# Kernel optimization log

Hardware: AMD Instinct MI355X
Metric: run time of the kernel (lower is better)

Reference implementation:

```python
import jax, jax.numpy as jnp
import numpy as np

N = 100000      # nodes
E = 320000      # edges
D = 128         # num_node_in_embeddings
DE = 256        # num_edge_in_embeddings = 2*D
NOBJ = 160
NREL = 27
BN_EPS = 1e-5   # eval-mode BatchNorm with running_mean=0, running_var=1


def setup_inputs() -> dict:
    key = jax.random.key(0)
    ks = jax.random.split(key, 24)
    f32 = jnp.float32
    def rn(k, shape, scale=0.05):
        return jax.random.normal(k, shape, f32) * scale
    return {
        "node_feats": jax.random.normal(ks[0], (N, D), f32),
        "edge_index": jax.random.randint(ks[1], (E, 2), 0, N),
        # GCNConv layers (W: [in,out], bias)
        "gcn1_W": rn(ks[2], (D, D // 2)), "gcn1_b": rn(ks[3], (D // 2,)),
        "gcn2_W": rn(ks[4], (D // 2, D)), "gcn2_b": rn(ks[5], (D,)),
        # edge attention (Linear(DE, D//2))
        "eattn_W": rn(ks[6], (DE, D // 2)), "eattn_b": rn(ks[7], (D // 2,)),
        # node attention (Linear(D, DE//2)) and indicator reduction (Linear(DE, DE//2))
        "nattn_W": rn(ks[8], (D, DE // 2)), "nattn_b": rn(ks[9], (DE // 2,)),
        "nred_W": rn(ks[10], (DE, DE // 2)), "nred_b": rn(ks[11], (DE // 2,)),
        # edge MLPs (1x1 Conv1d == Linear)
        "emlp1_W": rn(ks[12], (DE, DE // 2)), "emlp1_b": rn(ks[13], (DE // 2,)),
        "emlp2_W": rn(ks[14], (DE // 2, DE)), "emlp2_b": rn(ks[15], (DE,)),
        # node classification head
        "nlin1_W": rn(ks[16], (D, D // 2)),
        "nbn_g": jnp.ones((D // 2,), f32) + rn(ks[17], (D // 2,)),
        "nbn_b": rn(ks[18], (D // 2,)),
        "nlin2_W": rn(ks[19], (D // 2, NOBJ)),
        # edge classification head
        "elin1_W": rn(ks[20], (DE, DE // 2)),
        "ebn_g": jnp.ones((DE // 2,), f32) + rn(ks[21], (DE // 2,)),
        "ebn_b": rn(ks[22], (DE // 2,)),
        "elin2_W": rn(ks[23], (DE // 2, NREL)),
    }


def _seg_mean(vals, idx, n):
    # torch_scatter 'mean': sum / clamp(count, 1)
    s = jax.ops.segment_sum(vals, idx, num_segments=n)
    c = jax.ops.segment_sum(jnp.ones((vals.shape[0], 1), vals.dtype), idx, num_segments=n)
    return s / jnp.maximum(c, 1.0)


def _gcn_conv(x, src, dst, W, b, n):
    # PyG GCNConv, add_self_loops=True, symmetric normalization.
    lin = x @ W
    deg = jax.ops.segment_sum(jnp.ones((src.shape[0],), x.dtype), dst, num_segments=n) + 1.0
    dis = jax.lax.rsqrt(deg)                       # deg^{-1/2}, includes self-loop
    norm = dis[src] * dis[dst]                     # per-edge norm
    agg = jax.ops.segment_sum(lin[src] * norm[:, None], dst, num_segments=n)
    return agg + lin * (dis * dis)[:, None] + b    # self-loop term + bias


def _bn_eval(x, g, b):
    # eval-mode BatchNorm1d with running_mean=0, running_var=1
    return x * (g / jnp.sqrt(1.0 + BN_EPS)) + b


def reference(node_feats, edge_index, gcn1_W, gcn1_b, gcn2_W, gcn2_b,
              eattn_W, eattn_b, nattn_W, nattn_b, nred_W, nred_b,
              emlp1_W, emlp1_b, emlp2_W, emlp2_b,
              nlin1_W, nbn_g, nbn_b, nlin2_W,
              elin1_W, ebn_g, ebn_b, elin2_W):
    n = node_feats.shape[0]
    src = edge_index[:, 0]
    dst = edge_index[:, 1]

    # edge feature init: [subject, object - subject]  -> [E, DE]
    subj = node_feats[src]
    edge_feats = jnp.concatenate([subj, node_feats[dst] - subj], axis=1)

    # edge attention -> scatter-mean indicators over rows/cols -> node gate
    edge_ind = edge_feats @ eattn_W + eattn_b            # [E, D/2]
    row = _seg_mean(edge_ind, src, n)                    # [N, D/2]
    col = _seg_mean(edge_ind, dst, n)                    # [N, D/2]
    agg_edge_indicator = jax.nn.sigmoid(row * col)

    # two GCN layers (dropout is identity in eval mode)
    h = jax.nn.relu(_gcn_conv(node_feats, src, dst, gcn1_W, gcn1_b, n)) * agg_edge_indicator
    h = jax.nn.relu(_gcn_conv(h, src, dst, gcn2_W, gcn2_b, n))           # [N, D]

    # node attention -> per-edge gate
    node_ind = jax.nn.relu(h @ nattn_W + nattn_b)                        # [N, DE/2]
    econcat = jnp.concatenate([node_ind[src], node_ind[dst]], axis=1)    # [E, DE]
    agg_node_indicator = jax.nn.sigmoid(econcat @ nred_W + nred_b)       # [E, DE/2]

    # edge MLPs (1x1 convs == linears over edges)
    ef = jax.nn.relu(edge_feats @ emlp1_W + emlp1_b) * agg_node_indicator
    ef = jax.nn.relu(ef @ emlp2_W + emlp2_b)                             # [E, DE]

    # node head: linear -> BN(eval) -> leaky_relu(0.2) -> linear -> softmax over classes
    nx = jax.nn.leaky_relu(_bn_eval(h @ nlin1_W, nbn_g, nbn_b), 0.2)
    node_logits = jax.nn.softmax(nx @ nlin2_W, axis=1)                   # [N, NOBJ]

    # edge head: note original applies softmax on dim=1 of [1,E,NREL] -> over EDGES
    ex = jax.nn.leaky_relu(_bn_eval(ef @ elin1_W, ebn_g, ebn_b), 0.2)
    edge_logits = jax.nn.softmax(ex @ elin2_W, axis=0)                   # [E, NREL]

    return (node_logits, edge_logits)
```

## Files before the change

### kernel.cpp

```cpp
#include <hip/hip_runtime.h>

#define NN 100000
#define EE 320000

typedef unsigned int uint32;
typedef __attribute__((ext_vector_type(8))) short bf16x8;
typedef __attribute__((ext_vector_type(4))) float f32x4;
typedef __attribute__((ext_vector_type(16))) float f32x16;

__device__ __forceinline__ float4 ld4(const float* p){ return *(const float4*)p; }
__device__ __forceinline__ void st4(float* p, const float4 v){ *(float4*)p = v; }
__device__ __forceinline__ float sigm(float x){ return 1.f/(1.f + expf(-x)); }
__device__ __forceinline__ short f2b(float f){
  union { float f; uint32 u; } v; v.f = f;
  uint32 r = (v.u + 0x7FFFu + ((v.u>>16)&1u)) >> 16;
  return (short)r;
}

constexpr int EM_STORE=0, EM_BRELU=1, EM_BNLK=2;

template<int K,int NOUT,int EM>
__global__ __launch_bounds__(256) void gemm_k(
    const float* __restrict__ A,
    const float* __restrict__ W, const float* __restrict__ bias,
    const float* __restrict__ bng,
    float* __restrict__ C, int M)
{
  constexpr int CN = NOUT/16;
  __shared__ float As[16][68];
  __shared__ float Ws[16][NOUT];
  const int t  = threadIdx.x;
  const int tx = t & 15, ty = t >> 4;
  const int row0 = blockIdx.x * 64;

  float acc[4][CN];
  #pragma unroll
  for (int i=0;i<4;i++)
    #pragma unroll
    for (int j=0;j<CN;j++) acc[i][j]=0.f;

  const int r_st  = t >> 2;
  const int kq_st = (t & 3) * 4;

  for (int k0=0;k0<K;k0+=16) {
    {
      float4 v = make_float4(0.f,0.f,0.f,0.f);
      const int gr = row0 + r_st;
      if (gr < M) v = ld4(A + (size_t)gr*K + k0 + kq_st);
      As[kq_st+0][r_st]=v.x; As[kq_st+1][r_st]=v.y;
      As[kq_st+2][r_st]=v.z; As[kq_st+3][r_st]=v.w;
    }
    {
      constexpr int C4 = NOUT/4;
      for (int i=t;i<16*C4;i+=256){ int kk=i/C4, c4=(i%C4)*4;
        st4(&Ws[kk][c4], ld4(W + (size_t)(k0+kk)*NOUT + c4)); }
    }
    __syncthreads();
    #pragma unroll
    for (int kk=0;kk<16;kk++){
      float a0,a1,a2,a3;
      { const float4 av = *(const float4*)&As[kk][ty*4]; a0=av.x;a1=av.y;a2=av.z;a3=av.w; }
      float b[CN];
      if constexpr ((CN & 3) == 0) {
        #pragma unroll
        for (int j4=0;j4<CN;j4+=4){
          const float4 bv = *(const float4*)&Ws[kk][tx*CN+j4];
          b[j4]=bv.x;b[j4+1]=bv.y;b[j4+2]=bv.z;b[j4+3]=bv.w; }
      } else {
        #pragma unroll
        for (int j=0;j<CN;j++) b[j]=Ws[kk][tx*CN+j];
      }
      #pragma unroll
      for (int j=0;j<CN;j++){
        acc[0][j]=fmaf(a0,b[j],acc[0][j]);
        acc[1][j]=fmaf(a1,b[j],acc[1][j]);
        acc[2][j]=fmaf(a2,b[j],acc[2][j]);
        acc[3][j]=fmaf(a3,b[j],acc[3][j]);
      }
    }
    __syncthreads();
  }

  float sc[CN], sh[CN];
  if constexpr (EM==EM_BNLK) {
    const float r_ = rsqrtf(1.f + 1e-5f);
    #pragma unroll
    for (int j=0;j<CN;j++){ int c=tx*CN+j; sc[j]=bng[c]*r_; sh[j]=bias[c]; }
  }
  #pragma unroll
  for (int i=0;i<4;i++){
    const int r  = row0 + ty*4+i;
    if (r >= M) continue;
    #pragma unroll
    for (int j=0;j<CN;j++){
      const int c = tx*CN+j;
      float v = acc[i][j];
      if constexpr (EM==EM_BRELU) v = fmaxf(v + bias[c], 0.f);
      else if constexpr (EM==EM_BNLK){ float x = fmaf(v, sc[j], sh[j]); v = (x>0.f)? x : 0.2f*x; }
      C[(size_t)r*NOUT + c] = v;
    }
  }
}

__global__ void k_hist(const int* __restrict__ eidx, int* cntS, int* cntD, int E){
  int e = blockIdx.x*256+threadIdx.x; if (e>=E) return;
  atomicAdd(&cntS[eidx[2*e]], 1);
  atomicAdd(&cntD[eidx[2*e+1]], 1);
}
__global__ void k_scan_sum(const int* __restrict__ cnt, int* bsum, int n){
  __shared__ int red[256];
  const int b=blockIdx.x, t=threadIdx.x;
  int s=0;
  for (int i=b*1024+t; i<n && i<(b+1)*1024; i+=256) s += cnt[i];
  red[t]=s; __syncthreads();
  for (int o=128;o;o>>=1){ if(t<o) red[t]+=red[t+o]; __syncthreads(); }
  if (t==0) bsum[b]=red[0];
}
__global__ void k_scan_top(int* bsum, int nb){
  __shared__ int sh[256];
  const int t=threadIdx.x;
  int v=(t<nb)?bsum[t]:0;
  sh[t]=v; __syncthreads();
  for (int o=1;o<256;o<<=1){
    int u=0; if(t>=o) u=sh[t-o];
    __syncthreads();
    sh[t]+=u;
    __syncthreads();
  }
  if (t<nb) bsum[t]=sh[t]-v;
}
__global__ void k_scan_out(const int* __restrict__ cnt, const int* __restrict__ bofs,
                           int* __restrict__ off, int n){
  __shared__ int sh[256];
  const int b=blockIdx.x, t=threadIdx.x;
  const int base=b*1024+t*4;
  int c0=0,c1=0,c2=0,c3=0;
  if(base+0<n)c0=cnt[base+0];
  if(base+1<n)c1=cnt[base+1];
  if(base+2<n)c2=cnt[base+2];
  if(base+3<n)c3=cnt[base+3];
  int s=c0+c1+c2+c3;
  sh[t]=s; __syncthreads();
  int v=s;
  for (int o=1;o<256;o<<=1){
    int u=0; if(t>=o) u=sh[t-o];
    __syncthreads();
    sh[t]+=u;
    __syncthreads();
  }
  const int tofs = sh[t]-v + bofs[b];
  if(base+0<n) off[base+0]=tofs;
  if(base+1<n) off[base+1]=tofs+c0;
  if(base+2<n) off[base+2]=tofs+c0+c1;
  if(base+3<n) off[base+3]=tofs+c0+c1+c2;
}
__global__ void k_copyoff(const int* __restrict__ off, int* __restrict__ cur, int n){
  int i=blockIdx.x*256+threadIdx.x;
  if (i<n) cur[i]=off[i];
}
__global__ void k_setend(int* offS, int* offD, int n, int E){
  if (threadIdx.x==0 && blockIdx.x==0){ offS[n]=E; offD[n]=E; }
}
__global__ void k_fill(const int* __restrict__ eidx, int* curS, int* curD,
                       int* __restrict__ csrS, int* __restrict__ csrD, int E){
  int e=blockIdx.x*256+threadIdx.x; if (e>=E) return;
  const int s=eidx[2*e], d=eidx[2*e+1];
  csrS[atomicAdd(&curS[s],1)] = d;
  csrD[atomicAdd(&curD[d],1)] = s;
}
__global__ void k_dis(const int* __restrict__ cntD, float* __restrict__ dis, int n){
  int i=blockIdx.x*256+threadIdx.x; if(i>=n)return;
  dis[i]=rsqrtf((float)cntD[i]+1.f);
}

__global__ void k_wprep(const float* __restrict__ eattnW, const float* __restrict__ gcn1W,
                        float* __restrict__ Wcat){
  int idx=blockIdx.x*256+threadIdx.x; if (idx>=128*192) return;
  int k=idx/192, c=idx-k*192;
  float v;
  if (c<64)       v = eattnW[(size_t)(128+k)*64 + c];
  else if (c<128) v = eattnW[(size_t)k*64 + (c-64)] - eattnW[(size_t)(128+k)*64 + (c-64)];
  else            v = gcn1W[(size_t)k*64 + (c-128)];
  Wcat[idx]=v;
}

template<int NC>
__global__ void k_gather(const float* __restrict__ src, int stride, int colbase,
                         const int* __restrict__ off, const int* __restrict__ csr,
                         float* __restrict__ out, int n){
  constexpr int TPN = NC/4;
  const int t=threadIdx.x;
  const int node = blockIdx.x*(256/TPN) + t/TPN; if (node>=n) return;
  const int cq = (t%TPN)*4;
  const int j1=off[node+1];
  float4 acc = make_float4(0.f,0.f,0.f,0.f);
  for (int j=off[node]; j<j1; ++j){
    const float4 v = ld4(src + (size_t)csr[j]*stride + colbase + cq);
    acc.x+=v.x; acc.y+=v.y; acc.z+=v.z; acc.w+=v.w;
  }
  st4(out + (size_t)node*NC + cq, acc);
}

__global__ void k_aei3(const float* __restrict__ TUL, const float* __restrict__ Q,
                       const float* __restrict__ S, const int* __restrict__ cntS,
                       const int* __restrict__ cntD, const float* __restrict__ bias,
                       float* __restrict__ aei, int n){
  int idx=blockIdx.x*256+threadIdx.x; if (idx>=n*16) return;
  const int i=idx>>4, cq=(idx&15)*4;
  const float cS=(float)cntS[i], cD=(float)cntD[i];
  const float iS=1.f/fmaxf(cS,1.f), iD=1.f/fmaxf(cD,1.f);
  const float* tul = TUL + (size_t)i*192;
  const float4 T4=ld4(tul+cq), U4=ld4(tul+64+cq);
  const float4 Q4=ld4(Q+(size_t)i*64+cq), S4=ld4(S+(size_t)i*64+cq), b4=ld4(bias+cq);
  float4 o;
  o.x=sigm(((cS*(U4.x+b4.x)+Q4.x)*iS) * ((cD*(T4.x+b4.x)+S4.x)*iD));
  o.y=sigm(((cS*(U4.y+b4.y)+Q4.y)*iS) * ((cD*(T4.y+b4.y)+S4.y)*iD));
  o.z=sigm(((cS*(U4.z+b4.z)+Q4.z)*iS) * ((cD*(T4.z+b4.z)+S4.z)*iD));
  o.w=sigm(((cS*(U4.w+b4.w)+Q4.w)*iS) * ((cD*(T4.w+b4.w)+S4.w)*iD));
  st4(aei + (size_t)i*64 + cq, o);
}

template<int NC, bool AEI>
__global__ void k_gcnagg(const float* __restrict__ lin, int stride, int colbase,
                         const int* __restrict__ off, const int* __restrict__ csr,
                         const float* __restrict__ dis, const float* __restrict__ aei,
                         const float* __restrict__ bias, float* __restrict__ h, int n){
  constexpr int TPN = NC/4;
  const int t=threadIdx.x;
  const int node = blockIdx.x*(256/TPN) + t/TPN; if (node>=n) return;
  const int cq = (t%TPN)*4;
  const int j1=off[node+1];
  float4 acc = make_float4(0.f,0.f,0.f,0.f);
  for (int j=off[node]; j<j1; ++j){
    const int s=csr[j];
    const float w=dis[s];
    const float4 v = ld4(lin + (size_t)s*stride + colbase + cq);
    acc.x=fmaf(v.x,w,acc.x); acc.y=fmaf(v.y,w,acc.y);
    acc.z=fmaf(v.z,w,acc.z); acc.w=fmaf(v.w,w,acc.w);
  }
  const float dn=dis[node], d2=dn*dn;
  const float4 own=ld4(lin + (size_t)node*stride + colbase + cq), b4=ld4(bias+cq);
  float4 o;
  o.x=fmaxf(fmaf(acc.x,dn,fmaf(own.x,d2,b4.x)),0.f);
  o.y=fmaxf(fmaf(acc.y,dn,fmaf(own.y,d2,b4.y)),0.f);
  o.z=fmaxf(fmaf(acc.z,dn,fmaf(own.z,d2,b4.z)),0.f);
  o.w=fmaxf(fmaf(acc.w,dn,fmaf(own.w,d2,b4.w)),0.f);
  if (AEI){ const float4 m=ld4(aei+(size_t)node*NC+cq); o.x*=m.x;o.y*=m.y;o.z*=m.z;o.w*=m.w; }
  st4(h + (size_t)node*NC + cq, o);
}

__global__ void k_twt(const float* __restrict__ W, short* __restrict__ Wt,
                      int K, int N, int NP, int krot){
  int idx = blockIdx.x*256 + threadIdx.x;
  if (idx >= NP*K) return;
  int n = idx / K, k = idx - n*K;
  int ks = k + krot; if (ks >= K) ks -= K;
  Wt[idx] = (n<N)? f2b(W[(size_t)ks*N + n]) : (short)0;
}

template<int KTOT, int NT>
__device__ __forceinline__ void mm32(
    const short* __restrict__ Wt,
    short (*As)[264], short (*Bs)[128][24],
    int t, int lane, int w, f32x16* acc)
{
  constexpr int STEPS = KTOT/16;
  constexpr int NC = NT*32;
  const int lane31 = lane & 31, kh = lane >> 5;
  const int arow = w*32 + lane31;
  const bool act = (t < NC*2);
  const int col = t >> 1, half = t & 1;
  const short* wp = Wt + (size_t)col*KTOT + half*8;
  float4 r;
  if (act){
    r = *(const float4*)wp;
    *(float4*)&Bs[0][col][half*8] = r;
  }
  __syncthreads();
  #pragma unroll
  for (int ks=0; ks<STEPS; ++ks){
    if (act && ks+1<STEPS) r = *(const float4*)(wp + (ks+1)*16);
    const bf16x8 a = *(const bf16x8*)&As[arow][ks*16 + kh*8];
    #pragma unroll
    for (int ct=0; ct<NT; ++ct){
      const bf16x8 b = *(const bf16x8*)&Bs[ks&1][ct*32 + lane31][kh*8];
      acc[ct] = __builtin_amdgcn_mfma_f32_32x32x16_bf16(a, b, acc[ct], 0, 0, 0);
    }
    if (act && ks+1<STEPS) *(float4*)&Bs[(ks+1)&1][col][half*8] = r;
    __syncthreads();
  }
}

__device__ __forceinline__ int rowof(int reg, int kh){
  return (reg & 3) + ((reg >> 2) << 3) + (kh << 2);
}

__global__ __launch_bounds__(256) void k_edge(
  const float* __restrict__ nf, const float* __restrict__ ni,
  const int* __restrict__ eidx,
  const short* __restrict__ wt_nred, const float* __restrict__ nredb,
  const short* __restrict__ wt_e1,   const float* __restrict__ e1b,
  const short* __restrict__ wt_e2,   const float* __restrict__ e2b,
  const short* __restrict__ wt_l1,   const float* __restrict__ ebng, const float* __restrict__ ebnb,
  const short* __restrict__ wt_l2,
  float* __restrict__ elog)
{
  __shared__ short As[128][264];
  __shared__ short Bs[2][128][24];
  const int t = threadIdx.x;
  const int lane = t & 63, w = t >> 6;
  const int row0 = blockIdx.x * 128;
  const int lane31 = lane & 31, kh = lane >> 5;

  const int srow = t >> 1, sseg = t & 1;
  const int s_s = eidx[2*(row0+srow)], s_d = eidx[2*(row0+srow)+1];

  {
    const float* src = sseg ? (ni + (size_t)s_d*128) : (ni + (size_t)s_s*128);
    short* dst = &As[srow][sseg*128];
    #pragma unroll
    for (int p=0;p<16;p++){
      float4 u = ld4(src + p*8), v = ld4(src + p*8 + 4);
      bf16x8 o;
      o[0]=f2b(u.x);o[1]=f2b(u.y);o[2]=f2b(u.z);o[3]=f2b(u.w);
      o[4]=f2b(v.x);o[5]=f2b(v.y);o[6]=f2b(v.z);o[7]=f2b(v.w);
      *(bf16x8*)(dst + p*8) = o;
    }
  }
  f32x16 acc[4];
  #pragma unroll
  for (int j=0;j<4;j++) acc[j] = (f32x16)(0.f);
  mm32<256,4>(wt_nred, As, Bs, t, lane, w, acc);

  uint32 gp[4][8];
  #pragma unroll
  for (int ct=0;ct<4;ct++){
    const float bb = nredb[ct*32 + lane31];
    #pragma unroll
    for (int rq=0;rq<8;rq++){
      const uint32 g0 = (uint32)(unsigned short)f2b(sigm(acc[ct][2*rq]   + bb));
      const uint32 g1 = (uint32)(unsigned short)f2b(sigm(acc[ct][2*rq+1] + bb));
      gp[ct][rq] = g0 | (g1<<16);
    }
  }

  {
    short* dst = &As[srow][sseg*128];
    #pragma unroll
    for (int p=0;p<16;p++){
      float4 u, v;
      if (sseg == 0){
        u = ld4(nf + (size_t)s_s*128 + p*8);
        v = ld4(nf + (size_t)s_s*128 + p*8 + 4);
      } else {
        float4 ua = ld4(nf + (size_t)s_d*128 + p*8);
        float4 ub = ld4(nf + (size_t)s_s*128 + p*8);
        float4 va = ld4(nf + (size_t)s_d*128 + p*8 + 4);
        float4 vb = ld4(nf + (size_t)s_s*128 + p*8 + 4);
        u.x=ua.x-ub.x; u.y=ua.y-ub.y; u.z=ua.z-ub.z; u.w=ua.w-ub.w;
        v.x=va.x-vb.x; v.y=va.y-vb.y; v.z=va.z-vb.z; v.w=va.w-vb.w;
      }
      bf16x8 o;
      o[0]=f2b(u.x);o[1]=f2b(u.y);o[2]=f2b(u.z);o[3]=f2b(u.w);
      o[4]=f2b(v.x);o[5]=f2b(v.y);o[6]=f2b(v.z);o[7]=f2b(v.w);
      *(bf16x8*)(dst + p*8) = o;
    }
  }
  #pragma unroll
  for (int j=0;j<4;j++) acc[j] = (f32x16)(0.f);
  mm32<256,4>(wt_e1, As, Bs, t, lane, w, acc);

  #pragma unroll
  for (int ct=0;ct<4;ct++){
    const int col = ct*32 + lane31;
    const float bb = e1b[col];
    #pragma unroll
    for (int reg=0;reg<16;reg++){
      const uint32 u = gp[ct][reg>>1];
      const float gv = __uint_as_float((reg&1) ? (u & 0xFFFF0000u) : (u<<16));
      As[w*32 + rowof(reg,kh)][col] = f2b(fmaxf(acc[ct][reg] + bb, 0.f) * gv);
    }
  }

  #pragma unroll
  for (int j=0;j<4;j++) acc[j] = (f32x16)(0.f);
  mm32<128,4>(wt_e2, As, Bs, t, lane, w, acc);
  #pragma unroll
  for (int ct=0;ct<4;ct++){
    const int col = ct*32 + lane31;
    const float bb = e2b[col];
    #pragma unroll
    for (int reg=0;reg<16;reg++)
      As[w*32 + rowof(reg,kh)][128+col] = f2b(fmaxf(acc[ct][reg] + bb, 0.f));
  }
  #pragma unroll
  for (int j=0;j<4;j++) acc[j] = (f32x16)(0.f);
  mm32<128,4>(wt_e2 + (size_t)128*128, As, Bs, t, lane, w, acc);
  #pragma unroll
  for (int ct=0;ct<4;ct++){
    const int col = ct*32 + lane31;
    const float bb = e2b[128+col];
    #pragma unroll
    for (int reg=0;reg<16;reg++)
      As[w*32 + rowof(reg,kh)][col] = f2b(fmaxf(acc[ct][reg] + bb, 0.f));
  }

  #pragma unroll
  for (int j=0;j<4;j++) acc[j] = (f32x16)(0.f);
  mm32<256,4>(wt_l1, As, Bs, t, lane, w, acc);
  {
    const float r_ = rsqrtf(1.f + 1e-5f);
    #pragma unroll
    for (int ct=0;ct<4;ct++){
      const int col = ct*32 + lane31;
      const float sc = ebng[col]*r_, sh = ebnb[col];
      #pragma unroll
      for (int reg=0;reg<16;reg++){
        float x = fmaf(acc[ct][reg], sc, sh);
        As[w*32 + rowof(reg,kh)][col] = f2b((x>0.f)? x : 0.2f*x);
      }
    }
  }

  f32x16 acc5 = (f32x16)(0.f);
  mm32<128,1>(wt_l2, As, Bs, t, lane, w, &acc5);

  float* Lb = (float*)&As[0][0];
  if (lane31 < 27){
    #pragma unroll
    for (int reg=0;reg<16;reg++)
      Lb[(w*32 + rowof(reg,kh))*28 + lane31] = acc5[reg];
  }
  __syncthreads();
  for (int i=t; i<128*27; i+=256){
    int rr = i/27, cc = i - rr*27;
    elog[(size_t)(row0+rr)*27 + cc] = Lb[rr*28 + cc];
  }
}

__global__ __launch_bounds__(256) void k_softmax_row(float* __restrict__ x, int M){
  const int wave = threadIdx.x>>6, lane = threadIdx.x&63;
  const int r = blockIdx.x*4 + wave; if (r>=M) return;
  float* p = x + (size_t)r*160;
  float v0 = p[lane], v1 = p[64+lane];
  float v2 = (lane<32)? p[128+lane] : -3.4e38f;
  float m = fmaxf(fmaxf(v0,v1),v2);
  for (int o=32;o;o>>=1) m = fmaxf(m, __shfl_xor(m,o));
  float e0=expf(v0-m), e1=expf(v1-m), e2=(lane<32)?expf(v2-m):0.f;
  float s=e0+e1+e2;
  for (int o=32;o;o>>=1) s += __shfl_xor(s,o);
  float inv = 1.f/s;
  p[lane]=e0*inv; p[64+lane]=e1*inv; if(lane<32)p[128+lane]=e2*inv;
}
__global__ void k_colmax(const float* __restrict__ x, uint32* __restrict__ cmax_u, int E){
  __shared__ float red[8][32];
  const int t=threadIdx.x, col=t&31, seg=t>>5;
  float m = -3.4e38f;
  if (col < 27)
    for (int r = blockIdx.x*8 + seg; r < E; r += gridDim.x*8)
      m = fmaxf(m, x[(size_t)r*27+col]);
  red[seg][col]=m; __syncthreads();
  if (t<32){
    float mm=red[0][t];
    #pragma unroll
    for (int s2=1;s2<8;s2++) mm=fmaxf(mm,red[s2][t]);
    if (t<27){
      uint32 u=__float_as_uint(mm);
      u = (u&0x80000000u)? ~u : (u|0x80000000u);
      atomicMax(&cmax_u[t], u);
    }
  }
}
__global__ void k_colfix(const uint32* __restrict__ cmax_u, float* __restrict__ cmaxf){
  int t=threadIdx.x; if (t>=27) return;
  uint32 u=cmax_u[t];
  cmaxf[t] = (u&0x80000000u)? __uint_as_float(u&0x7FFFFFFFu) : __uint_as_float(~u);
}
__global__ void k_colsum(const float* __restrict__ x, const float* __restrict__ cmaxf,
                         float* __restrict__ csum, int E){
  __shared__ float red[8][32];
  const int t=threadIdx.x, col=t&31, seg=t>>5;
  float s = 0.f;
  if (col < 27){
    const float cm = cmaxf[col];
    for (int r = blockIdx.x*8 + seg; r < E; r += gridDim.x*8)
      s += expf(x[(size_t)r*27+col] - cm);
  }
  red[seg][col]=s; __syncthreads();
  if (t<32){
    float ss=red[0][t];
    #pragma unroll
    for (int s2=1;s2<8;s2++) ss+=red[s2][t];
    if (t<27) atomicAdd(&csum[t], ss);
  }
}
__global__ void k_colnorm(float* __restrict__ x, const float* __restrict__ cmaxf,
                          const float* __restrict__ csum, int E){
  int idx=blockIdx.x*256+threadIdx.x;
  if (idx >= E*27) return;
  int c = idx - (idx/27)*27;
  x[idx] = expf(x[idx]-cmaxf[c]) / csum[c];
}

extern "C" void kernel_launch(void* const* d_in, const int* in_sizes, int n_in,
                              void* d_out, int out_size, void* d_ws, size_t ws_size,
                              hipStream_t stream)
{
  const float* nf     = (const float*)d_in[0];
  const int*   eidx   = (const int*)  d_in[1];
  const float* gcn1W  = (const float*)d_in[2];
  const float* gcn1b  = (const float*)d_in[3];
  const float* gcn2W  = (const float*)d_in[4];
  const float* gcn2b  = (const float*)d_in[5];
  const float* eattnW = (const float*)d_in[6];
  const float* eattnb = (const float*)d_in[7];
  const float* nattnW = (const float*)d_in[8];
  const float* nattnb = (const float*)d_in[9];
  const float* nredW  = (const float*)d_in[10];
  const float* nredb  = (const float*)d_in[11];
  const float* emlp1W = (const float*)d_in[12];
  const float* emlp1b = (const float*)d_in[13];
  const float* emlp2W = (const float*)d_in[14];
  const float* emlp2b = (const float*)d_in[15];
  const float* nlin1W = (const float*)d_in[16];
  const float* nbng   = (const float*)d_in[17];
  const float* nbnb   = (const float*)d_in[18];
  const float* nlin2W = (const float*)d_in[19];
  const float* elin1W = (const float*)d_in[20];
  const float* ebng   = (const float*)d_in[21];
  const float* ebnb   = (const float*)d_in[22];
  const float* elin2W = (const float*)d_in[23];
  (void)in_sizes; (void)n_in; (void)out_size; (void)ws_size;

  const int N = NN, E = EE;
  float* out  = (float*)d_out;
  float* nlog = out;
  float* elog = out + (size_t)N*160;

  float* ws   = (float*)d_ws;
  float* h2   = ws;
  float* lin2 = ws + (size_t)N*128;
  float* Q    = lin2;
  float* S    = lin2 + (size_t)N*64;
  float* niB  = lin2;
  float* nx   = lin2;
  float* TUL  = ws + (size_t)N*256;
  float* h1   = ws + (size_t)N*448;
  float* aei  = ws + (size_t)N*512;
  float* dis  = ws + (size_t)N*576;
  float* smalls = ws + (size_t)N*577;
  float* Wcat = smalls + 128;
  int*   ip   = (int*)(Wcat + 24576);
  int* cntS = ip;
  int* cntD = ip + N;
  int* offS = ip + 2*N;
  int* offD = ip + 3*N + 64;
  int* curS = ip + 4*N + 128;
  int* curD = ip + 5*N + 128;
  int* csrS = ip + 6*N + 128;
  int* csrD = ip + 6*N + 128 + E;
  int* bsum = ip + 6*N + 128 + 2*E;
  short* wtb  = (short*)(bsum + 256);
  short* wt_nred = wtb;
  short* wt_e1   = wtb + 32768;
  short* wt_e2   = wtb + 65536;
  short* wt_l1   = wtb + 98304;
  short* wt_l2   = wtb + 131072;

  const int NB1024 = (N + 1023)/1024;

  k_twt<<<128,256,0,stream>>>(nredW,  wt_nred, 256, 128, 128, 0);
  k_twt<<<128,256,0,stream>>>(emlp1W, wt_e1,   256, 128, 128, 0);
  k_twt<<<128,256,0,stream>>>(emlp2W, wt_e2,   128, 256, 256, 0);
  k_twt<<<128,256,0,stream>>>(elin1W, wt_l1,   256, 128, 128, 128);
  k_twt<<<16, 256,0,stream>>>(elin2W, wt_l2,   128, 27,  32,  0);
  k_wprep<<<96,256,0,stream>>>(eattnW, gcn1W, Wcat);

  (void)hipMemsetAsync(cntS, 0, 2*(size_t)N*sizeof(int), stream);
  k_hist<<<(E+255)/256,256,0,stream>>>(eidx, cntS, cntD, E);
  k_scan_sum<<<NB1024,256,0,stream>>>(cntS, bsum, N);
  k_scan_top<<<1,256,0,stream>>>(bsum, NB1024);
  k_scan_out<<<NB1024,256,0,stream>>>(cntS, bsum, offS, N);
  k_scan_sum<<<NB1024,256,0,stream>>>(cntD, bsum, N);
  k_scan_top<<<1,256,0,stream>>>(bsum, NB1024);
  k_scan_out<<<NB1024,256,0,stream>>>(cntD, bsum, offD, N);
  k_setend<<<1,64,0,stream>>>(offS, offD, N, E);
  k_copyoff<<<(N+255)/256,256,0,stream>>>(offS, curS, N);
  k_copyoff<<<(N+255)/256,256,0,stream>>>(offD, curD, N);
  k_fill<<<(E+255)/256,256,0,stream>>>(eidx, curS, curD, csrS, csrD, E);
  k_dis<<<(N+255)/256,256,0,stream>>>(cntD, dis, N);

  gemm_k<128,192,EM_STORE><<<(N+63)/64,256,0,stream>>>(nf, Wcat, nullptr, nullptr, TUL, N);

  k_gather<64><<<(N+15)/16,256,0,stream>>>(TUL, 192, 0,  offS, csrS, Q, N);
  k_gather<64><<<(N+15)/16,256,0,stream>>>(TUL, 192, 64, offD, csrD, S, N);
  k_aei3<<<(N*16+255)/256,256,0,stream>>>(TUL, Q, S, cntS, cntD, eattnb, aei, N);

  k_gcnagg<64,true><<<(N+15)/16,256,0,stream>>>(TUL, 192, 128, offD, csrD, dis, aei, gcn1b, h1, N);

  gemm_k<64,128,EM_STORE><<<(N+63)/64,256,0,stream>>>(h1, gcn2W, nullptr, nullptr, lin2, N);
  k_gcnagg<128,false><<<(N+7)/8,256,0,stream>>>(lin2, 128, 0, offD, csrD, dis, nullptr, gcn2b, h2, N);

  gemm_k<128,128,EM_BRELU><<<(N+63)/64,256,0,stream>>>(h2, nattnW, nattnb, nullptr, niB, N);

  k_edge<<<E/128,256,0,stream>>>(
      nf, niB, eidx,
      wt_nred, nredb, wt_e1, emlp1b, wt_e2, emlp2b,
      wt_l1, ebng, ebnb, wt_l2, elog);

  gemm_k<128,64,EM_BNLK><<<(N+63)/64,256,0,stream>>>(h2, nlin1W, nbnb, nbng, nx, N);
  gemm_k<64,160,EM_STORE><<<(N+63)/64,256,0,stream>>>(nx, nlin2W, nullptr, nullptr, nlog, N);
  k_softmax_row<<<(N+3)/4,256,0,stream>>>(nlog, N);

  (void)hipMemsetAsync(smalls, 0, 96*sizeof(float), stream);
  k_colmax<<<1024,256,0,stream>>>(elog, (uint32*)smalls, E);
  k_colfix<<<1,32,0,stream>>>((const uint32*)smalls, smalls+64);
  k_colsum<<<1024,256,0,stream>>>(elog, smalls+64, smalls+32, E);
  k_colnorm<<<(E*27+255)/256,256,0,stream>>>(elog, smalls+64, smalls+32, E);
}
```

Baseline: 975.4 us.

## Precompute per-node projections for edge gate and first edge MLP layer

Splits the two edge-level linear layers on concatenated node features (nred on [ni_src, ni_dst], emlp1 on [nf_src, nf_dst-nf_src]) into per-node projections computed once per node in a new k_pa kernel. The edge kernel then gathers bf16 projected rows, adds them with the biases, and applies the sigmoid/relu gating, dropping two K=256 MFMA GEMMs per edge tile. The aim is to cut edge-level matmul work roughly 3.2x for those layers, at the cost of an extra node kernel and bf16 rounding of the partial sums. mm32 also loses its register-prefetch double buffering of B in favour of a single shared buffer with two barriers per k-step, which may add stalls.

```diff
diff --git a/kernel.cpp b/kernel.cpp
--- a/kernel.cpp
+++ b/kernel.cpp
@@ -15,6 +15,9 @@
   union { float f; uint32 u; } v; v.f = f;
   uint32 r = (v.u + 0x7FFFu + ((v.u>>16)&1u)) >> 16;
   return (short)r;
+}
+__device__ __forceinline__ float b2f(short s){
+  union { uint32 u; float f; } v; v.u = ((uint32)(unsigned short)s) << 16; return v.f;
 }
 
 constexpr int EM_STORE=0, EM_BRELU=1, EM_BNLK=2;
@@ -249,19 +252,24 @@
   st4(h + (size_t)node*NC + cq, o);
 }
 
-__global__ void k_twt(const float* __restrict__ W, short* __restrict__ Wt,
-                      int K, int N, int NP, int krot){
+__global__ void k_twtg(const float* __restrict__ Wa, const float* __restrict__ Wb,
+                       short* __restrict__ Wt, int K, int N, int NP, int rowoff, int krot){
   int idx = blockIdx.x*256 + threadIdx.x;
   if (idx >= NP*K) return;
-  int n = idx / K, k = idx - n*K;
+  int nn = idx / K, k = idx - nn*K;
   int ks = k + krot; if (ks >= K) ks -= K;
-  Wt[idx] = (n<N)? f2b(W[(size_t)ks*N + n]) : (short)0;
+  float v = 0.f;
+  if (nn < N){
+    v = Wa[(size_t)(ks+rowoff)*N + nn];
+    if (Wb) v -= Wb[(size_t)(ks+rowoff)*N + nn];
+  }
+  Wt[idx] = f2b(v);
 }
 
 template<int KTOT, int NT>
 __device__ __forceinline__ void mm32(
     const short* __restrict__ Wt,
-    short (*As)[264], short (*Bs)[128][24],
+    short (*As)[258], short (*Bs)[28],
     int t, int lane, int w, f32x16* acc)
 {
   constexpr int STEPS = KTOT/16;
@@ -271,22 +279,16 @@
   const bool act = (t < NC*2);
   const int col = t >> 1, half = t & 1;
   const short* wp = Wt + (size_t)col*KTOT + half*8;
-  float4 r;
-  if (act){
-    r = *(const float4*)wp;
-    *(float4*)&Bs[0][col][half*8] = r;
-  }
-  __syncthreads();
   #pragma unroll
   for (int ks=0; ks<STEPS; ++ks){
-    if (act && ks+1<STEPS) r = *(const float4*)(wp + (ks+1)*16);
+    if (act) *(float4*)&Bs[col][half*8] = *(const float4*)(wp + ks*16);
+    __syncthreads();
     const bf16x8 a = *(const bf16x8*)&As[arow][ks*16 + kh*8];
     #pragma unroll
     for (int ct=0; ct<NT; ++ct){
-      const bf16x8 b = *(const bf16x8*)&Bs[ks&1][ct*32 + lane31][kh*8];
+      const bf16x8 b = *(const bf16x8*)&Bs[ct*32 + lane31][kh*8];
       acc[ct] = __builtin_amdgcn_mfma_f32_32x32x16_bf16(a, b, acc[ct], 0, 0, 0);
     }
-    if (act && ks+1<STEPS) *(float4*)&Bs[(ks+1)&1][col][half*8] = r;
     __syncthreads();
   }
 }
@@ -295,95 +297,133 @@
   return (reg & 3) + ((reg >> 2) << 3) + (kh << 2);
 }
 
+__device__ __forceinline__ void storePA(short* __restrict__ dst, int cb, int n0, int n,
+                                        int w, int kh, int lane31, const f32x16* acc){
+  #pragma unroll
+  for (int ct=0;ct<4;ct++){
+    #pragma unroll
+    for (int reg=0;reg<16;reg++){
+      const int rr = n0 + w*32 + rowof(reg,kh);
+      if (rr < n) dst[(size_t)rr*256 + cb + ct*32 + lane31] = f2b(acc[ct][reg]);
+    }
+  }
+}
+
+__global__ __launch_bounds__(256) void k_pa(
+  const float* __restrict__ niB, const float* __restrict__ nf,
+  const short* __restrict__ wt_p1, const short* __restrict__ wt_p2,
+  const short* __restrict__ wt_a1, const short* __restrict__ wt_a2,
+  short* __restrict__ PAs, short* __restrict__ PAd, int n)
+{
+  __shared__ short As[128][258];
+  __shared__ short Bs[128][28];
+  const int t = threadIdx.x, lane = t & 63, w = t >> 6;
+  const int lane31 = lane & 31, kh = lane >> 5;
+  const int n0 = blockIdx.x * 128;
+  const int srow = t >> 1, shalf = t & 1;
+  const int grow = n0 + srow;
+
+  {
+    short* dst = &As[srow][shalf*64];
+    if (grow < n){
+      const float* src = niB + (size_t)grow*128 + shalf*64;
+      #pragma unroll
+      for (int p=0;p<8;p++){
+        float4 u=ld4(src+p*8), v=ld4(src+p*8+4);
+        bf16x8 o;
+        o[0]=f2b(u.x);o[1]=f2b(u.y);o[2]=f2b(u.z);o[3]=f2b(u.w);
+        o[4]=f2b(v.x);o[5]=f2b(v.y);o[6]=f2b(v.z);o[7]=f2b(v.w);
+        *(bf16x8*)(dst+p*8)=o;
+      }
+    } else {
+      #pragma unroll
+      for (int p=0;p<8;p++) *(bf16x8*)(dst+p*8) = (bf16x8)0;
+    }
+  }
+  f32x16 acc[4];
+  #pragma unroll
+  for (int j=0;j<4;j++) acc[j]=(f32x16)(0.f);
+  mm32<128,4>(wt_p1, As, Bs, t, lane, w, acc);
+  storePA(PAs, 0, n0, n, w, kh, lane31, acc);
+  #pragma unroll
+  for (int j=0;j<4;j++) acc[j]=(f32x16)(0.f);
+  mm32<128,4>(wt_p2, As, Bs, t, lane, w, acc);
+  storePA(PAd, 0, n0, n, w, kh, lane31, acc);
+  __syncthreads();
+
+  {
+    short* dst = &As[srow][shalf*64];
+    if (grow < n){
+      const float* src = nf + (size_t)grow*128 + shalf*64;
+      #pragma unroll
+      for (int p=0;p<8;p++){
+        float4 u=ld4(src+p*8), v=ld4(src+p*8+4);
+        bf16x8 o;
+        o[0]=f2b(u.x);o[1]=f2b(u.y);o[2]=f2b(u.z);o[3]=f2b(u.w);
+        o[4]=f2b(v.x);o[5]=f2b(v.y);o[6]=f2b(v.z);o[7]=f2b(v.w);
+        *(bf16x8*)(dst+p*8)=o;
+      }
+    } else {
+      #pragma unroll
+      for (int p=0;p<8;p++) *(bf16x8*)(dst+p*8) = (bf16x8)0;
+    }
+  }
+  #pragma unroll
+  for (int j=0;j<4;j++) acc[j]=(f32x16)(0.f);
+  mm32<128,4>(wt_a1, As, Bs, t, lane, w, acc);
+  storePA(PAs, 128, n0, n, w, kh, lane31, acc);
+  #pragma unroll
+  for (int j=0;j<4;j++) acc[j]=(f32x16)(0.f);
+  mm32<128,4>(wt_a2, As, Bs, t, lane, w, acc);
+  storePA(PAd, 128, n0, n, w, kh, lane31, acc);
+}
+
 __global__ __launch_bounds__(256) void k_edge(
-  const float* __restrict__ nf, const float* __restrict__ ni,
+  const short* __restrict__ PAs, const short* __restrict__ PAd,
   const int* __restrict__ eidx,
-  const short* __restrict__ wt_nred, const float* __restrict__ nredb,
-  const short* __restrict__ wt_e1,   const float* __restrict__ e1b,
-  const short* __restrict__ wt_e2,   const float* __restrict__ e2b,
-  const short* __restrict__ wt_l1,   const float* __restrict__ ebng, const float* __restrict__ ebnb,
+  const float* __restrict__ nredb, const float* __restrict__ e1b,
+  const short* __restrict__ wt_e2, const float* __restrict__ e2b,
+  const short* __restrict__ wt_l1, const float* __restrict__ ebng, const float* __restrict__ ebnb,
   const short* __restrict__ wt_l2,
   float* __restrict__ elog)
 {
-  __shared__ short As[128][264];
-  __shared__ short Bs[2][128][24];
-  const int t = threadIdx.x;
-  const int lane = t & 63, w = t >> 6;
+  __shared__ short As[128][258];
+  __shared__ short Bs[128][28];
+  const int t = threadIdx.x, lane = t & 63, w = t >> 6;
+  const int lane31 = lane & 31, kh = lane >> 5;
   const int row0 = blockIdx.x * 128;
-  const int lane31 = lane & 31, kh = lane >> 5;
-
-  const int srow = t >> 1, sseg = t & 1;
-  const int s_s = eidx[2*(row0+srow)], s_d = eidx[2*(row0+srow)+1];
 
   {
-    const float* src = sseg ? (ni + (size_t)s_d*128) : (ni + (size_t)s_s*128);
-    short* dst = &As[srow][sseg*128];
-    #pragma unroll
-    for (int p=0;p<16;p++){
-      float4 u = ld4(src + p*8), v = ld4(src + p*8 + 4);
+    const int srow = t >> 1, sseg = t & 1;
+    const int e = row0 + srow;
+    const int s = eidx[2*e], d = eidx[2*e+1];
+    const short* ps = PAs + (size_t)s*256;
+    const short* pd = PAd + (size_t)d*256;
+    #pragma unroll
+    for (int c0=0;c0<64;c0+=8){
+      const int c = sseg*64 + c0;
+      const bf16x8 p1 = *(const bf16x8*)(ps + c);
+      const bf16x8 p2 = *(const bf16x8*)(pd + c);
+      const bf16x8 a1 = *(const bf16x8*)(ps + 128 + c);
+      const bf16x8 a2 = *(const bf16x8*)(pd + 128 + c);
+      const float4 bg0=ld4(nredb+c), bg1=ld4(nredb+c+4);
+      const float4 be0=ld4(e1b+c),   be1=ld4(e1b+c+4);
+      const float bg[8]={bg0.x,bg0.y,bg0.z,bg0.w,bg1.x,bg1.y,bg1.z,bg1.w};
+      const float be[8]={be0.x,be0.y,be0.z,be0.w,be1.x,be1.y,be1.z,be1.w};
       bf16x8 o;
-      o[0]=f2b(u.x);o[1]=f2b(u.y);o[2]=f2b(u.z);o[3]=f2b(u.w);
-      o[4]=f2b(v.x);o[5]=f2b(v.y);o[6]=f2b(v.z);o[7]=f2b(v.w);
-      *(bf16x8*)(dst + p*8) = o;
-    }
-  }
+      #pragma unroll
+      for (int j=0;j<8;j++){
+        const float g = sigm(b2f(p1[j]) + b2f(p2[j]) + bg[j]);
+        const float v = fmaxf(b2f(a1[j]) + b2f(a2[j]) + be[j], 0.f) * g;
+        o[j] = f2b(v);
+      }
+      *(bf16x8*)&As[srow][c] = o;
+    }
+  }
+
   f32x16 acc[4];
   #pragma unroll
-  for (int j=0;j<4;j++) acc[j] = (f32x16)(0.f);
-  mm32<256,4>(wt_nred, As, Bs, t, lane, w, acc);
-
-  uint32 gp[4][8];
-  #pragma unroll
-  for (int ct=0;ct<4;ct++){
-    const float bb = nredb[ct*32 + lane31];
-    #pragma unroll
-    for (int rq=0;rq<8;rq++){
-      const uint32 g0 = (uint32)(unsigned short)f2b(sigm(acc[ct][2*rq]   + bb));
-      const uint32 g1 = (uint32)(unsigned short)f2b(sigm(acc[ct][2*rq+1] + bb));
-      gp[ct][rq] = g0 | (g1<<16);
-    }
-  }
-
-  {
-    short* dst = &As[srow][sseg*128];
-    #pragma unroll
-    for (int p=0;p<16;p++){
-      float4 u, v;
-      if (sseg == 0){
-        u = ld4(nf + (size_t)s_s*128 + p*8);
-        v = ld4(nf + (size_t)s_s*128 + p*8 + 4);
-      } else {
-        float4 ua = ld4(nf + (size_t)s_d*128 + p*8);
-        float4 ub = ld4(nf + (size_t)s_s*128 + p*8);
-        float4 va = ld4(nf + (size_t)s_d*128 + p*8 + 4);
-        float4 vb = ld4(nf + (size_t)s_s*128 + p*8 + 4);
-        u.x=ua.x-ub.x; u.y=ua.y-ub.y; u.z=ua.z-ub.z; u.w=ua.w-ub.w;
-        v.x=va.x-vb.x; v.y=va.y-vb.y; v.z=va.z-vb.z; v.w=va.w-vb.w;
-      }
-      bf16x8 o;
-      o[0]=f2b(u.x);o[1]=f2b(u.y);o[2]=f2b(u.z);o[3]=f2b(u.w);
-      o[4]=f2b(v.x);o[5]=f2b(v.y);o[6]=f2b(v.z);o[7]=f2b(v.w);
-      *(bf16x8*)(dst + p*8) = o;
-    }
-  }
-  #pragma unroll
-  for (int j=0;j<4;j++) acc[j] = (f32x16)(0.f);
-  mm32<256,4>(wt_e1, As, Bs, t, lane, w, acc);
-
-  #pragma unroll
-  for (int ct=0;ct<4;ct++){
-    const int col = ct*32 + lane31;
-    const float bb = e1b[col];
-    #pragma unroll
-    for (int reg=0;reg<16;reg++){
-      const uint32 u = gp[ct][reg>>1];
-      const float gv = __uint_as_float((reg&1) ? (u & 0xFFFF0000u) : (u<<16));
-      As[w*32 + rowof(reg,kh)][col] = f2b(fmaxf(acc[ct][reg] + bb, 0.f) * gv);
-    }
-  }
-
-  #pragma unroll
-  for (int j=0;j<4;j++) acc[j] = (f32x16)(0.f);
+  for (int j=0;j<4;j++) acc[j]=(f32x16)(0.f);
   mm32<128,4>(wt_e2, As, Bs, t, lane, w, acc);
   #pragma unroll
   for (int ct=0;ct<4;ct++){
@@ -394,7 +434,7 @@
       As[w*32 + rowof(reg,kh)][128+col] = f2b(fmaxf(acc[ct][reg] + bb, 0.f));
   }
   #pragma unroll
-  for (int j=0;j<4;j++) acc[j] = (f32x16)(0.f);
+  for (int j=0;j<4;j++) acc[j]=(f32x16)(0.f);
   mm32<128,4>(wt_e2 + (size_t)128*128, As, Bs, t, lane, w, acc);
   #pragma unroll
   for (int ct=0;ct<4;ct++){
@@ -406,7 +446,7 @@
   }
 
   #pragma unroll
-  for (int j=0;j<4;j++) acc[j] = (f32x16)(0.f);
+  for (int j=0;j<4;j++) acc[j]=(f32x16)(0.f);
   mm32<256,4>(wt_l1, As, Bs, t, lane, w, acc);
   {
     const float r_ = rsqrtf(1.f + 1e-5f);
@@ -416,7 +456,7 @@
       const float sc = ebng[col]*r_, sh = ebnb[col];
       #pragma unroll
       for (int reg=0;reg<16;reg++){
-        float x = fmaf(acc[ct][reg], sc, sh);
+        const float x = fmaf(acc[ct][reg], sc, sh);
         As[w*32 + rowof(reg,kh)][col] = f2b((x>0.f)? x : 0.2f*x);
       }
     }
@@ -546,6 +586,8 @@
   float* nx   = lin2;
   float* TUL  = ws + (size_t)N*256;
   float* h1   = ws + (size_t)N*448;
+  short* PAs  = (short*)TUL;
+  short* PAd  = PAs + (size_t)N*256;
   float* aei  = ws + (size_t)N*512;
   float* dis  = ws + (size_t)N*576;
   float* smalls = ws + (size_t)N*577;
@@ -561,19 +603,23 @@
   int* csrD = ip + 6*N + 128 + E;
   int* bsum = ip + 6*N + 128 + 2*E;
   short* wtb  = (short*)(bsum + 256);
-  short* wt_nred = wtb;
-  short* wt_e1   = wtb + 32768;
-  short* wt_e2   = wtb + 65536;
-  short* wt_l1   = wtb + 98304;
-  short* wt_l2   = wtb + 131072;
+  short* wt_p1 = wtb;
+  short* wt_p2 = wtb + 16384;
+  short* wt_a1 = wtb + 32768;
+  short* wt_a2 = wtb + 49152;
+  short* wt_e2 = wtb + 65536;
+  short* wt_l1 = wtb + 98304;
+  short* wt_l2 = wtb + 131072;
 
   const int NB1024 = (N + 1023)/1024;
 
-  k_twt<<<128,256,0,stream>>>(nredW,  wt_nred, 256, 128, 128, 0);
-  k_twt<<<128,256,0,stream>>>(emlp1W, wt_e1,   256, 128, 128, 0);
-  k_twt<<<128,256,0,stream>>>(emlp2W, wt_e2,   128, 256, 256, 0);
-  k_twt<<<128,256,0,stream>>>(elin1W, wt_l1,   256, 128, 128, 128);
-  k_twt<<<16, 256,0,stream>>>(elin2W, wt_l2,   128, 27,  32,  0);
+  k_twtg<<<64, 256,0,stream>>>(nredW,  nullptr, wt_p1, 128,128,128, 0,   0);
+  k_twtg<<<64, 256,0,stream>>>(nredW,  nullptr, wt_p2, 128,128,128, 128, 0);
+  k_twtg<<<64, 256,0,stream>>>(emlp1W, emlp1W+(size_t)128*128, wt_a1, 128,128,128, 0, 0);
+  k_twtg<<<64, 256,0,stream>>>(emlp1W, nullptr, wt_a2, 128,128,128, 128, 0);
+  k_twtg<<<128,256,0,stream>>>(emlp2W, nullptr, wt_e2, 128,256,256, 0,   0);
+  k_twtg<<<128,256,0,stream>>>(elin1W, nullptr, wt_l1, 256,128,128, 0, 128);
+  k_twtg<<<16, 256,0,stream>>>(elin2W, nullptr, wt_l2, 128,27, 32,  0,   0);
   k_wprep<<<96,256,0,stream>>>(eattnW, gcn1W, Wcat);
 
   (void)hipMemsetAsync(cntS, 0, 2*(size_t)N*sizeof(int), stream);
@@ -603,9 +649,11 @@
 
   gemm_k<128,128,EM_BRELU><<<(N+63)/64,256,0,stream>>>(h2, nattnW, nattnb, nullptr, niB, N);
 
+  k_pa<<<(N+127)/128,256,0,stream>>>(niB, nf, wt_p1, wt_p2, wt_a1, wt_a2, PAs, PAd, N);
+
   k_edge<<<E/128,256,0,stream>>>(
-      nf, niB, eidx,
-      wt_nred, nredb, wt_e1, emlp1b, wt_e2, emlp2b,
+      PAs, PAd, eidx,
+      nredb, emlp1b, wt_e2, emlp2b,
       wt_l1, ebng, ebnb, wt_l2, elog);
 
   gemm_k<128,64,EM_BNLK><<<(N+63)/64,256,0,stream>>>(h2, nlin1W, nbnb, nbng, nx, N);
```

Result: slower. 1.063 ms (+9.0%).
